# Performance work log

Measured on AMD Instinct MI355X. Metric: run time of the kernel, lower is better.

## Reference

```python
import jax, jax.numpy as jnp
import numpy as np


def setup_inputs() -> dict:
    key = jax.random.key(0)
    k1, k2, k3, k4, k5 = jax.random.split(key, 5)
    B, A, FI = 4096, 256, 16   # batch, atoms, iso functions per atom
    Bo, FA = 512, 8            # bonds, aniso functions per bond
    return {
        "c_iso": jax.random.normal(k1, (B, A, FI), dtype=jnp.float32),
        "c_aniso": jax.random.normal(k2, (B, Bo, FA), dtype=jnp.float32),
        "int_iso": jax.random.uniform(k3, (B, A, FI), dtype=jnp.float32),
        "int_aniso": jax.random.uniform(k4, (B, Bo, FA), dtype=jnp.float32),
        "charge": jax.random.normal(k5, (B, A), dtype=jnp.float32),
    }


def reference(c_iso, c_aniso, int_iso, int_aniso, charge):
    # Bordered KKT system from the Lagrangian L(x,u) = (x-c)^T(x-c) - u (q^T x - Q):
    #   q^T x     = Q
    # Exact closed-form solution (Sherman-Morrison on the rank-1 border):
    #   u = 2 (Q - q^T c) / (q^T q),   x = c + (u/2) q
    B = c_iso.shape[0]
    c = jnp.concatenate([c_iso.reshape(B, -1), c_aniso.reshape(B, -1)], axis=1)   # [B, n]
    q = jnp.concatenate([int_iso.reshape(B, -1), int_aniso.reshape(B, -1)], axis=1)  # [B, n]
    Q = jnp.sum(charge, axis=1)                                                   # [B]
    qTc = jnp.einsum("bn,bn->b", q, c)
    qTq = jnp.einsum("bn,bn->b", q, q)
    u = 2.0 * (Q - qTc) / qTq                                                     # Lagrange multiplier [B]
    x = c + 0.5 * u[:, None] * q                                                  # [B, n]
    n_iso = c_iso.shape[1] * c_iso.shape[2]
    sol_iso = x[:, :n_iso].reshape(c_iso.shape)
    sol_aniso = x[:, n_iso:].reshape(c_aniso.shape)
    return (sol_iso, sol_aniso)
```

## Files before the change

kernel.cpp:

```cpp
#include <hip/hip_runtime.h>


#define HALF_N 4096
#define BLOCK  256

__global__ __launch_bounds__(BLOCK, 4) void qp_charge_norm_kernel(
    const float* __restrict__ c_iso,
    const float* __restrict__ c_aniso,
    const float* __restrict__ q_iso,
    const float* __restrict__ q_aniso,
    const float* __restrict__ charge,
    float* __restrict__ out,
    int B)
{
    const int b   = blockIdx.x;
    const int tid = threadIdx.x;

    const float4* ci = (const float4*)(c_iso   + (size_t)b * HALF_N);
    const float4* ca = (const float4*)(c_aniso + (size_t)b * HALF_N);
    const float4* qi = (const float4*)(q_iso   + (size_t)b * HALF_N);
    const float4* qa = (const float4*)(q_aniso + (size_t)b * HALF_N);

    float4 cv[8], qv[8];
#pragma unroll
    for (int j = 0; j < 4; ++j) {
        cv[j]     = ci[j * BLOCK + tid];
        qv[j]     = qi[j * BLOCK + tid];
        cv[j + 4] = ca[j * BLOCK + tid];
        qv[j + 4] = qa[j * BLOCK + tid];
    }

    float qc = 0.0f, qq = 0.0f;
#pragma unroll
    for (int j = 0; j < 8; ++j) {
        qc += qv[j].x * cv[j].x + qv[j].y * cv[j].y
            + qv[j].z * cv[j].z + qv[j].w * cv[j].w;
        qq += qv[j].x * qv[j].x + qv[j].y * qv[j].y
            + qv[j].z * qv[j].z + qv[j].w * qv[j].w;
    }
    float Qp = charge[(size_t)b * 256 + tid];

#pragma unroll
    for (int off = 32; off > 0; off >>= 1) {
        qc += __shfl_down(qc, off, 64);
        qq += __shfl_down(qq, off, 64);
        Qp += __shfl_down(Qp, off, 64);
    }

    __shared__ float s_qc[4], s_qq[4], s_Q[4];
    __shared__ float s_half_u;
    const int wave = tid >> 6;
    const int lane = tid & 63;
    if (lane == 0) { s_qc[wave] = qc; s_qq[wave] = qq; s_Q[wave] = Qp; }
    __syncthreads();
    if (tid == 0) {
        float tqc = s_qc[0] + s_qc[1] + s_qc[2] + s_qc[3];
        float tqq = s_qq[0] + s_qq[1] + s_qq[2] + s_qq[3];
        float tQ  = s_Q[0]  + s_Q[1]  + s_Q[2]  + s_Q[3];
        s_half_u = (tQ - tqc) / tqq;
    }
    __syncthreads();
    const float h = s_half_u;

    float4* oi = (float4*)(out + (size_t)b * HALF_N);
    float4* oa = (float4*)(out + (size_t)B * HALF_N + (size_t)b * HALF_N);
#pragma unroll
    for (int j = 0; j < 4; ++j) {
        float4 r;
        r.x = cv[j].x + h * qv[j].x;
        r.y = cv[j].y + h * qv[j].y;
        r.z = cv[j].z + h * qv[j].z;
        r.w = cv[j].w + h * qv[j].w;
        oi[j * BLOCK + tid] = r;

        float4 s;
        s.x = cv[j + 4].x + h * qv[j + 4].x;
        s.y = cv[j + 4].y + h * qv[j + 4].y;
        s.z = cv[j + 4].z + h * qv[j + 4].z;
        s.w = cv[j + 4].w + h * qv[j + 4].w;
        oa[j * BLOCK + tid] = s;
    }
}

extern "C" void kernel_launch(void* const* d_in, const int* in_sizes, int n_in,
                              void* d_out, int out_size, void* d_ws, size_t ws_size,
                              hipStream_t stream) {
    const float* c_iso   = (const float*)d_in[0];
    const float* c_aniso = (const float*)d_in[1];
    const float* q_iso   = (const float*)d_in[2];
    const float* q_aniso = (const float*)d_in[3];
    const float* charge  = (const float*)d_in[4];
    float* out = (float*)d_out;

    const int B = in_sizes[0] / HALF_N;

    qp_charge_norm_kernel<<<B, BLOCK, 0, stream>>>(
        c_iso, c_aniso, q_iso, q_aniso, charge, out, B);
}
```

Baseline: 320.8 us.

## Use 512-thread blocks with fewer registers per thread and nontemporal output stores

Doubles the block size to 512 threads, so each thread holds 4 vectors of c and q instead of 8. This lowers register pressure and allows more waves resident per CU. Output writes become nontemporal stores so the streaming output does not pollute cache, and an empty asm barrier keeps the loaded values in registers. The charge load is masked to the first 256 threads, and the cross-wave reduction now spans 8 waves.

```diff
diff --git a/kernel.cpp b/kernel.cpp
--- a/kernel.cpp
+++ b/kernel.cpp
@@ -2,9 +2,11 @@
 
 
 #define HALF_N 4096
-#define BLOCK  256
+#define BLOCK  512
 
-__global__ __launch_bounds__(BLOCK, 4) void qp_charge_norm_kernel(
+typedef float f4 __attribute__((ext_vector_type(4)));
+
+__global__ __launch_bounds__(BLOCK, 8) void qp_charge_norm_kernel(
     const float* __restrict__ c_iso,
     const float* __restrict__ c_aniso,
     const float* __restrict__ q_iso,
@@ -16,29 +18,35 @@
     const int b   = blockIdx.x;
     const int tid = threadIdx.x;
 
-    const float4* ci = (const float4*)(c_iso   + (size_t)b * HALF_N);
-    const float4* ca = (const float4*)(c_aniso + (size_t)b * HALF_N);
-    const float4* qi = (const float4*)(q_iso   + (size_t)b * HALF_N);
-    const float4* qa = (const float4*)(q_aniso + (size_t)b * HALF_N);
+    const f4* ci = (const f4*)(c_iso   + (size_t)b * HALF_N);
+    const f4* ca = (const f4*)(c_aniso + (size_t)b * HALF_N);
+    const f4* qi = (const f4*)(q_iso   + (size_t)b * HALF_N);
+    const f4* qa = (const f4*)(q_aniso + (size_t)b * HALF_N);
 
-    float4 cv[8], qv[8];
+    f4 cv[4], qv[4];
 #pragma unroll
-    for (int j = 0; j < 4; ++j) {
+    for (int j = 0; j < 2; ++j) {
         cv[j]     = ci[j * BLOCK + tid];
         qv[j]     = qi[j * BLOCK + tid];
-        cv[j + 4] = ca[j * BLOCK + tid];
-        qv[j + 4] = qa[j * BLOCK + tid];
+        cv[j + 2] = ca[j * BLOCK + tid];
+        qv[j + 2] = qa[j * BLOCK + tid];
     }
 
     float qc = 0.0f, qq = 0.0f;
 #pragma unroll
-    for (int j = 0; j < 8; ++j) {
-        qc += qv[j].x * cv[j].x + qv[j].y * cv[j].y
-            + qv[j].z * cv[j].z + qv[j].w * cv[j].w;
-        qq += qv[j].x * qv[j].x + qv[j].y * qv[j].y
-            + qv[j].z * qv[j].z + qv[j].w * qv[j].w;
+    for (int j = 0; j < 4; ++j) {
+        qc += qv[j][0] * cv[j][0] + qv[j][1] * cv[j][1]
+            + qv[j][2] * cv[j][2] + qv[j][3] * cv[j][3];
+        qq += qv[j][0] * qv[j][0] + qv[j][1] * qv[j][1]
+            + qv[j][2] * qv[j][2] + qv[j][3] * qv[j][3];
     }
-    float Qp = charge[(size_t)b * 256 + tid];
+
+#pragma unroll
+    for (int j = 0; j < 4; ++j) {
+        asm volatile("" : "+v"(cv[j]), "+v"(qv[j]));
+    }
+
+    float Qp = (tid < 256) ? charge[(size_t)b * 256 + tid] : 0.0f;
 
 #pragma unroll
     for (int off = 32; off > 0; off >>= 1) {
@@ -47,38 +55,29 @@
         Qp += __shfl_down(Qp, off, 64);
     }
 
-    __shared__ float s_qc[4], s_qq[4], s_Q[4];
+    __shared__ float s_qc[8], s_qq[8], s_Q[8];
     __shared__ float s_half_u;
     const int wave = tid >> 6;
     const int lane = tid & 63;
     if (lane == 0) { s_qc[wave] = qc; s_qq[wave] = qq; s_Q[wave] = Qp; }
     __syncthreads();
     if (tid == 0) {
-        float tqc = s_qc[0] + s_qc[1] + s_qc[2] + s_qc[3];
-        float tqq = s_qq[0] + s_qq[1] + s_qq[2] + s_qq[3];
-        float tQ  = s_Q[0]  + s_Q[1]  + s_Q[2]  + s_Q[3];
+        float tqc = 0.0f, tqq = 0.0f, tQ = 0.0f;
+#pragma unroll
+        for (int w = 0; w < 8; ++w) { tqc += s_qc[w]; tqq += s_qq[w]; tQ += s_Q[w]; }
         s_half_u = (tQ - tqc) / tqq;
     }
     __syncthreads();
     const float h = s_half_u;
 
-    float4* oi = (float4*)(out + (size_t)b * HALF_N);
-    float4* oa = (float4*)(out + (size_t)B * HALF_N + (size_t)b * HALF_N);
+    f4* oi = (f4*)(out + (size_t)b * HALF_N);
+    f4* oa = (f4*)(out + (size_t)B * HALF_N + (size_t)b * HALF_N);
 #pragma unroll
-    for (int j = 0; j < 4; ++j) {
-        float4 r;
-        r.x = cv[j].x + h * qv[j].x;
-        r.y = cv[j].y + h * qv[j].y;
-        r.z = cv[j].z + h * qv[j].z;
-        r.w = cv[j].w + h * qv[j].w;
-        oi[j * BLOCK + tid] = r;
-
-        float4 s;
-        s.x = cv[j + 4].x + h * qv[j + 4].x;
-        s.y = cv[j + 4].y + h * qv[j + 4].y;
-        s.z = cv[j + 4].z + h * qv[j + 4].z;
-        s.w = cv[j + 4].w + h * qv[j + 4].w;
-        oa[j * BLOCK + tid] = s;
+    for (int j = 0; j < 2; ++j) {
+        f4 r = cv[j]     + h * qv[j];
+        f4 s = cv[j + 2] + h * qv[j + 2];
+        __builtin_nontemporal_store(r, &oi[j * BLOCK + tid]);
+        __builtin_nontemporal_store(s, &oa[j * BLOCK + tid]);
     }
 }
 
```

Result: slower. 332.1 us (+3.5%).
